# Kernel optimization log

Hardware: AMD Instinct MI355X
Metric: run time of the kernel (lower is better)

The kernel has to match this reference:

```python
import jax, jax.numpy as jnp
import numpy as np

NUM_HEADS = 16
EPS = 1e-12  # matches torch F.normalize eps


def _l2norm(t):
    n = jnp.sqrt(jnp.sum(t * t, axis=-1, keepdims=True))
    return t / jnp.maximum(n, EPS)


def setup_inputs() -> dict:
    key = jax.random.key(0)
    kx, kq, kk, kv = jax.random.split(key, 4)
    B, S, E = 2, 2048, 1024
    head_dim = E // NUM_HEADS
    bound = 1.0 / np.sqrt(E)  # nn.Linear default init range
    x = jax.random.normal(kx, (B, S, E), dtype=jnp.float32)
    Wq = jax.random.uniform(kq, (E, E), dtype=jnp.float32, minval=-bound, maxval=bound)
    Wk = jax.random.uniform(kk, (E, E), dtype=jnp.float32, minval=-bound, maxval=bound)
    Wv = jax.random.uniform(kv, (E, E), dtype=jnp.float32, minval=-bound, maxval=bound)
    g_scale = jnp.asarray(np.sqrt(head_dim), dtype=jnp.float32)  # 1/d_k = sqrt(head_dim)
    return {"x": x, "Wq": Wq, "Wk": Wk, "Wv": Wv, "g_scale": g_scale}


def reference(x, Wq, Wk, Wv, g_scale):
    B, S, E = x.shape
    H = NUM_HEADS
    D = E // H
    # projections (torch Linear: x @ W.T), split heads -> [B, H, S, D]
    q = (x @ Wq.T).reshape(B, S, H, D).transpose(0, 2, 1, 3)
    k = (x @ Wk.T).reshape(B, S, H, D).transpose(0, 2, 1, 3)
    v = (x @ Wv.T).reshape(B, S, H, D).transpose(0, 2, 1, 3)
    # qk_norm branch: L2-normalize q, k then learnable scale
    q = _l2norm(q)
    k = _l2norm(k)
    scores = g_scale * jnp.einsum('bhqd,bhkd->bhqk', q, k)  # [B, H, S, S]
    attn = jax.nn.softmax(scores, axis=-1)
    # dropout p=0.0 (eval) -> identity
    out = jnp.einsum('bhqk,bhkd->bhqd', attn, v)  # [B, H, S, D]
    out = out.transpose(0, 2, 1, 3).reshape(B, S, E)
    return out
```

## Files before the change

### kernel.cpp

```cpp
#include <hip/hip_runtime.h>
#include <math.h>

#define NH 16
#define HD 64
#define SEQ 2048
#define BAT 2
#define EMB 1024
#define MTOT (BAT*SEQ)
#define NTOT (3*EMB)

typedef __attribute__((ext_vector_type(8))) short bf16x8;
typedef __attribute__((ext_vector_type(4))) float f32x4;

#define MFMA16(a,b,c) __builtin_amdgcn_mfma_f32_16x16x32_bf16(a,b,c,0,0,0)

__device__ inline short f2bf(float f) {
    union { float f; unsigned u; } x; x.f = f;
    unsigned r = (x.u + 0x7FFF + ((x.u >> 16) & 1)) >> 16;
    return (short)r;
}

__device__ inline float fast_exp2(float x) {
#if __has_builtin(__builtin_amdgcn_exp2f)
    return __builtin_amdgcn_exp2f(x);
#else
    float r; asm("v_exp_f32 %0, %1" : "=v"(r) : "v"(x)); return r;
#endif
}

__device__ inline unsigned pack2bf_t(float a, float b) {
    union { float f; unsigned u; } x, y; x.f = a; y.f = b;
    return __builtin_amdgcn_perm(y.u, x.u, 0x07060302u);
}

typedef const __attribute__((address_space(1))) void* gp_t;
typedef __attribute__((address_space(3))) void* lp_t;
__device__ inline void gload16(const void* g, void* l) {
    __builtin_amdgcn_global_load_lds((gp_t)(uintptr_t)g, (lp_t)(uintptr_t)l, 16, 0, 0);
}

__global__ __launch_bounds__(256) void prep_kernel(
    const float* __restrict__ x, const float* __restrict__ wq,
    const float* __restrict__ wk, const float* __restrict__ wv,
    short* __restrict__ xb, short* __restrict__ wb)
{
    const size_t NX = (size_t)MTOT * EMB;
    const size_t NW = (size_t)EMB * EMB;
    const size_t i4 = ((size_t)blockIdx.x * 256 + threadIdx.x) * 4;
    float4 v; short* dst;
    if (i4 < NX) { v = *(const float4*)(x + i4); dst = xb + i4; }
    else {
        size_t j = i4 - NX;
        const float* s = (j < NW) ? wq : (j < 2 * NW) ? wk : wv;
        v = *(const float4*)(s + (j & (NW - 1)));
        dst = wb + j;
    }
    short4 o; o.x = f2bf(v.x); o.y = f2bf(v.y); o.z = f2bf(v.z); o.w = f2bf(v.w);
    *(short4*)dst = o;
}

__global__ __launch_bounds__(256) void qkv_gemm_fast(
    const short* __restrict__ xb, const short* __restrict__ wb,
    short* __restrict__ qws, short* __restrict__ kws, short* __restrict__ vperm,
    const float* __restrict__ gptr)
{
    __shared__ short smem[2 * 2 * 128 * 64];
    const int m0 = blockIdx.x * 128, n0 = blockIdx.y * 128;
    const int t = threadIdx.x, wave = t >> 6, lane = t & 63;
    const int quad = lane >> 4, l16 = lane & 15;
    const int wm = (wave & 1) * 64, wn = (wave >> 1) * 64;

    const int srow = wave * 32 + (lane >> 3);
    const int scol = ((lane & 7) ^ (srow & 7)) * 8;
    const short* ga = xb + (size_t)(m0 + srow) * EMB + scol;
    const short* gb = wb + (size_t)(n0 + srow) * EMB + scol;

    int aoff[2], boff[2];
#pragma unroll
    for (int ks = 0; ks < 2; ++ks) {
        const int pc = (ks * 32 + quad * 8) ^ ((l16 & 7) * 8);
        aoff[ks] = (wm + l16) * 64 + pc;
        boff[ks] = 8192 + (wn + l16) * 64 + pc;
    }

    f32x4 acc[4][4] = {};

    auto stageg = [&](int k0, int p) {
        short* lA = smem + p * 16384 + wave * 2048;
        short* lB = smem + p * 16384 + 8192 + wave * 2048;
#pragma unroll
        for (int j = 0; j < 4; ++j) {
            gload16(ga + k0 + (size_t)j * 8 * EMB, lA + j * 512);
            gload16(gb + k0 + (size_t)j * 8 * EMB, lB + j * 512);
        }
    };

    stageg(0, 0);
    __syncthreads();

    for (int it = 0; it < EMB / 64; ++it) {
        const int p = it & 1;
        if (it + 1 < EMB / 64) stageg((it + 1) * 64, p ^ 1);
        const short* base = smem + p * 16384;
#pragma unroll
        for (int ks = 0; ks < 2; ++ks) {
            bf16x8 af[4], bfr[4];
#pragma unroll
            for (int i = 0; i < 4; ++i) af[i]  = *(const bf16x8*)(base + aoff[ks] + i * 1024);
#pragma unroll
            for (int i = 0; i < 4; ++i) bfr[i] = *(const bf16x8*)(base + boff[ks] + i * 1024);
#pragma unroll
            for (int mf = 0; mf < 4; ++mf)
#pragma unroll
                for (int nf = 0; nf < 4; ++nf)
                    acc[mf][nf] = MFMA16(af[mf], bfr[nf], acc[mf][nf]);
        }
        __syncthreads();
    }

    short* T = smem;
    const int mat = n0 >> 10;

    if (mat < 2) {
        const float scale = (mat == 0) ? gptr[0] * 1.4426950408889634f : 1.0f;
        float inv[4][4];
#pragma unroll
        for (int mf = 0; mf < 4; ++mf)
#pragma unroll
            for (int reg = 0; reg < 4; ++reg) {
                float ss = 0.f;
#pragma unroll
                for (int nf = 0; nf < 4; ++nf) { float v = acc[mf][nf][reg]; ss += v * v; }
                ss += __shfl_xor(ss, 1, 16);
                ss += __shfl_xor(ss, 2, 16);
                ss += __shfl_xor(ss, 4, 16);
                ss += __shfl_xor(ss, 8, 16);
                inv[mf][reg] = scale / fmaxf(sqrtf(ss), 1e-12f);
            }
#pragma unroll
        for (int mf = 0; mf < 4; ++mf)
#pragma unroll
            for (int nf = 0; nf < 4; ++nf) {
                const int c = wn + nf * 16 + l16;
#pragma unroll
                for (int reg = 0; reg < 4; ++reg) {
                    const int s = wm + mf * 16 + quad * 4 + reg;
                    T[s * 128 + (((c >> 3) ^ (s & 15)) << 3) + (c & 7)] =
                        f2bf(acc[mf][nf][reg] * inv[mf][reg]);
                }
            }
        __syncthreads();
        short* outp = (mat == 0) ? qws : kws;
        const int r = t >> 1, half = t & 1;
        const int sg = m0 + r, bb = sg >> 11, sl = sg & (SEQ - 1);
        const int h = ((n0 & 1023) >> 6) + half;
        short* orow = outp + ((size_t)(bb * NH + h) * SEQ + sl) * HD;
#pragma unroll
        for (int j = 0; j < 8; ++j) {
            int4 v = *(const int4*)&T[r * 128 + ((((half * 8 + j)) ^ (r & 15)) << 3)];
            *(int4*)&orow[j * 8] = v;
        }
    } else {
#pragma unroll
        for (int mf = 0; mf < 4; ++mf)
#pragma unroll
            for (int nf = 0; nf < 4; ++nf) {
                const int c = wn + nf * 16 + l16;
#pragma unroll
                for (int reg = 0; reg < 4; ++reg) {
                    const int s = wm + mf * 16 + quad * 4 + reg;
                    const int sp = (s & ~31) + ((s & 12) >> 2) * 8 + ((s >> 4) & 1) * 4 + (s & 3);
                    T[sp * 128 + (((c >> 3) ^ (sp & 15)) << 3) + (c & 7)] =
                        f2bf(acc[mf][nf][reg]);
                }
            }
        __syncthreads();
        const int c = t >> 1, half = t & 1;
        const int h = ((n0 & 1023) >> 6) + (c >> 6), d = c & 63;
        const int bb = m0 >> 11, p0 = (m0 & (SEQ - 1)) + half * 64;
        short* vrow = vperm + ((size_t)(bb * NH + h) * HD + d) * SEQ + p0;
        const int cg = c >> 3, ce = c & 7;
#pragma unroll
        for (int j = 0; j < 8; ++j) {
            union { int4 v; short s[8]; } tmp;
#pragma unroll
            for (int e = 0; e < 8; ++e) {
                const int s = half * 64 + j * 8 + e;
                tmp.s[e] = T[s * 128 + ((cg ^ (s & 15)) << 3) + ce];
            }
            *(int4*)&vrow[j * 8] = tmp.v;
        }
    }
}

__global__ __launch_bounds__(256, 4) void attn_kernel(
    const short* __restrict__ qws, const short* __restrict__ kws,
    const short* __restrict__ vperm, float* __restrict__ out)
{
    __shared__ short Kt[2][2][2048];
    __shared__ short Vt[2][2][2048];
    __shared__ float lbuf[64];

    const int id = blockIdx.x;
    const int bh = (id & 7) * 4 + ((id >> 3) & 3);
    const int qt = id >> 5;
    const int b = bh >> 4, h = bh & (NH - 1);
    const size_t base = (size_t)bh * SEQ * HD;
    const int t = threadIdx.x, wave = t >> 6, lane = t & 63;
    const int quad = lane >> 4, l16 = lane & 15;
    const int qh = wave >> 1, kh = wave & 1;

    bf16x8 bq[2][2];
#pragma unroll
    for (int qsub = 0; qsub < 2; ++qsub) {
        const short* qp = qws + base +
            (size_t)(qt * 64 + qh * 32 + qsub * 16 + l16) * HD + quad * 8;
        bq[qsub][0] = *(const bf16x8*)(qp);
        bq[qsub][1] = *(const bf16x8*)(qp + 32);
    }
    bf16x8 ones;
#pragma unroll
    for (int i = 0; i < 8; ++i) ones[i] = (short)0x3F80;

    int koff[2][2];
#pragma unroll
    for (int msub = 0; msub < 2; ++msub)
#pragma unroll
        for (int ks = 0; ks < 2; ++ks)
            koff[msub][ks] = (msub * 16 + l16) * 64 + (((ks * 4 + quad) ^ (l16 & 7)) * 8);
    int voff[4];
#pragma unroll
    for (int nt = 0; nt < 4; ++nt) {
        const int d = nt * 16 + l16;
        voff[nt] = d * 32 + ((quad ^ ((d >> 1) & 3)) * 8);
    }

    f32x4 o_acc[2][4] = {};
    f32x4 l_acc[2] = {};

    auto stage = [&](int tt, int p) {
        if (qh == 0) {
#pragma unroll
            for (int j = 0; j < 4; ++j) {
                const int kl = j * 8 + (lane >> 3);
                const int row = tt * 64 + kh * 32 + kl;
                gload16(kws + base + (size_t)row * HD + (((lane & 7) ^ (kl & 7)) * 8),
                        &Kt[p][kh][j * 512 + lane * 8]);
            }
        } else {
#pragma unroll
            for (int j = 0; j < 4; ++j) {
                const int d = j * 16 + (lane >> 2);
                const int ug = (lane & 3) ^ ((d >> 1) & 3);
                gload16(vperm + base + (size_t)d * SEQ + tt * 64 + kh * 32 + ug * 8,
                        &Vt[p][kh][j * 512 + lane * 8]);
            }
        }
    };

    stage(0, 0);
    __syncthreads();

    for (int tt = 0; tt < SEQ / 64; ++tt) {
        const int p = tt & 1;
        if (tt + 1 < SEQ / 64) stage(tt + 1, p ^ 1);
        const short* Kp = &Kt[p][kh][0];
        const short* Vp = &Vt[p][kh][0];

        f32x4 st[2][2];
#pragma unroll
        for (int msub = 0; msub < 2; ++msub) {
            bf16x8 a0 = *(const bf16x8*)(Kp + koff[msub][0]);
            bf16x8 a1 = *(const bf16x8*)(Kp + koff[msub][1]);
#pragma unroll
            for (int qsub = 0; qsub < 2; ++qsub) {
                f32x4 z = {};
                z = MFMA16(a0, bq[qsub][0], z);
                st[msub][qsub] = MFMA16(a1, bq[qsub][1], z);
            }
        }
        bf16x8 vf[4];
#pragma unroll
        for (int nt = 0; nt < 4; ++nt)
            vf[nt] = *(const bf16x8*)(Vp + voff[nt]);
#pragma unroll
        for (int qsub = 0; qsub < 2; ++qsub) {
            bf16x8 pa;
            unsigned* pu = (unsigned*)&pa;
            pu[0] = pack2bf_t(fast_exp2(st[0][qsub][0]), fast_exp2(st[0][qsub][1]));
            pu[1] = pack2bf_t(fast_exp2(st[0][qsub][2]), fast_exp2(st[0][qsub][3]));
            pu[2] = pack2bf_t(fast_exp2(st[1][qsub][0]), fast_exp2(st[1][qsub][1]));
            pu[3] = pack2bf_t(fast_exp2(st[1][qsub][2]), fast_exp2(st[1][qsub][3]));
            l_acc[qsub] = MFMA16(pa, ones, l_acc[qsub]);
#pragma unroll
            for (int nt = 0; nt < 4; ++nt)
                o_acc[qsub][nt] = MFMA16(pa, vf[nt], o_acc[qsub][nt]);
        }
        __syncthreads();
    }

    float* red = (float*)&Kt[0][0][0];
    if (kh == 1) {
#pragma unroll
        for (int qsub = 0; qsub < 2; ++qsub) {
#pragma unroll
            for (int nt = 0; nt < 4; ++nt)
#pragma unroll
                for (int r = 0; r < 4; ++r)
                    red[qh * 2048 + (qsub * 16 + quad * 4 + r) * 64 + nt * 16 + l16] =
                        o_acc[qsub][nt][r];
            if (l16 == 0)
#pragma unroll
                for (int r = 0; r < 4; ++r)
                    lbuf[qh * 32 + qsub * 16 + quad * 4 + r] = l_acc[qsub][r];
        }
    }
    __syncthreads();
    if (kh == 0) {
#pragma unroll
        for (int qsub = 0; qsub < 2; ++qsub) {
            float linv[4];
#pragma unroll
            for (int r = 0; r < 4; ++r)
                linv[r] = 1.0f / (l_acc[qsub][r] + lbuf[qh * 32 + qsub * 16 + quad * 4 + r]);
            const int s = qt * 64 + qh * 32 + qsub * 16 + quad * 4;
            float* ob = out + ((size_t)b * SEQ + s) * EMB + h * HD + l16;
#pragma unroll
            for (int nt = 0; nt < 4; ++nt)
#pragma unroll
                for (int r = 0; r < 4; ++r) {
                    const float o = o_acc[qsub][nt][r] +
                        red[qh * 2048 + (qsub * 16 + quad * 4 + r) * 64 + nt * 16 + l16];
                    ob[(size_t)r * EMB + nt * 16] = o * linv[r];
                }
        }
    }
}

extern "C" void kernel_launch(void* const* d_in, const int* in_sizes, int n_in,
                              void* d_out, int out_size, void* d_ws, size_t ws_size,
                              hipStream_t stream) {
    (void)in_sizes; (void)n_in; (void)out_size; (void)ws_size;
    const float* x  = (const float*)d_in[0];
    const float* Wq = (const float*)d_in[1];
    const float* Wk = (const float*)d_in[2];
    const float* Wv = (const float*)d_in[3];
    const float* g  = (const float*)d_in[4];
    float* out = (float*)d_out;

    const size_t per = (size_t)BAT * NH * SEQ * HD;
    short* qws   = (short*)d_ws;
    short* kws   = qws + per;
    short* vperm = kws + per;

    short* xb = (short*)out;
    short* wb = xb + (size_t)MTOT * EMB;

    prep_kernel<<<7168, 256, 0, stream>>>(x, Wq, Wk, Wv, xb, wb);
    qkv_gemm_fast<<<dim3(MTOT / 128, NTOT / 128), 256, 0, stream>>>(
        xb, wb, qws, kws, vperm, g);
    attn_kernel<<<(SEQ / 64) * BAT * NH, 256, 0, stream>>>(qws, kws, vperm, out);
}
```

Baseline: 161.6 us.

## Store bf16 operands in MFMA fragment-native tiled layout across all kernels

Changes the prep kernel, the QKV GEMM epilogue and the attention kernel so that x, weights, Q, K and V are stored in 16x32 fragment-blocked tiles matching the MFMA operand lane order. Global-to-LDS staging and LDS fragment reads then become plain contiguous lane*8 accesses, with no XOR swizzle or per-row address arithmetic. The goal is fewer address computations and fully contiguous 1KB loads. The cost is that LDS reads lose the swizzle and may hit bank conflicts, and the V epilogue scatter becomes more complex.

```diff
diff --git a/kernel.cpp b/kernel.cpp
--- a/kernel.cpp
+++ b/kernel.cpp
@@ -39,24 +39,33 @@
     __builtin_amdgcn_global_load_lds((gp_t)(uintptr_t)g, (lp_t)(uintptr_t)l, 16, 0, 0);
 }
 
+
 __global__ __launch_bounds__(256) void prep_kernel(
     const float* __restrict__ x, const float* __restrict__ wq,
     const float* __restrict__ wk, const float* __restrict__ wv,
     short* __restrict__ xb, short* __restrict__ wb)
 {
-    const size_t NX = (size_t)MTOT * EMB;
-    const size_t NW = (size_t)EMB * EMB;
-    const size_t i4 = ((size_t)blockIdx.x * 256 + threadIdx.x) * 4;
-    float4 v; short* dst;
-    if (i4 < NX) { v = *(const float4*)(x + i4); dst = xb + i4; }
-    else {
-        size_t j = i4 - NX;
-        const float* s = (j < NW) ? wq : (j < 2 * NW) ? wk : wv;
-        v = *(const float4*)(s + (j & (NW - 1)));
-        dst = wb + j;
-    }
-    short4 o; o.x = f2bf(v.x); o.y = f2bf(v.y); o.z = f2bf(v.z); o.w = f2bf(v.w);
-    *(short4*)dst = o;
+    const int g = blockIdx.x * 256 + threadIdx.x;
+    const int bid = g >> 6, lane = g & 63;
+    const int l16 = lane & 15, quad = lane >> 4;
+    const float* src; short* dst;
+    if (bid < 8192) {
+        const int S = bid >> 5, kb = bid & 31;
+        src = x + (size_t)(S * 16 + l16) * EMB + kb * 32 + quad * 8;
+        dst = xb + (size_t)bid * 512 + lane * 8;
+    } else {
+        const int wid = bid - 8192;
+        const int mat = wid >> 11, within = wid & 2047;
+        const int S = within >> 5, kb = within & 31;
+        const float* w = (mat == 0) ? wq : (mat == 1) ? wk : wv;
+        src = w + (size_t)(S * 16 + l16) * EMB + kb * 32 + quad * 8;
+        dst = wb + (size_t)wid * 512 + lane * 8;
+    }
+    float4 a = *(const float4*)src, b2 = *(const float4*)(src + 4);
+    union { int4 v; short s[8]; } o;
+    o.s[0]=f2bf(a.x);  o.s[1]=f2bf(a.y);  o.s[2]=f2bf(a.z);  o.s[3]=f2bf(a.w);
+    o.s[4]=f2bf(b2.x); o.s[5]=f2bf(b2.y); o.s[6]=f2bf(b2.z); o.s[7]=f2bf(b2.w);
+    *(int4*)dst = o.v;
 }
 
 __global__ __launch_bounds__(256) void qkv_gemm_fast(
@@ -64,34 +73,36 @@
     short* __restrict__ qws, short* __restrict__ kws, short* __restrict__ vperm,
     const float* __restrict__ gptr)
 {
-    __shared__ short smem[2 * 2 * 128 * 64];
+    __shared__ short smem[2 * 16384];
     const int m0 = blockIdx.x * 128, n0 = blockIdx.y * 128;
     const int t = threadIdx.x, wave = t >> 6, lane = t & 63;
     const int quad = lane >> 4, l16 = lane & 15;
     const int wm = (wave & 1) * 64, wn = (wave >> 1) * 64;
-
-    const int srow = wave * 32 + (lane >> 3);
-    const int scol = ((lane & 7) ^ (srow & 7)) * 8;
-    const short* ga = xb + (size_t)(m0 + srow) * EMB + scol;
-    const short* gb = wb + (size_t)(n0 + srow) * EMB + scol;
+    const int SA = m0 >> 4;
+    const int SB = n0 >> 4;
 
     int aoff[2], boff[2];
 #pragma unroll
     for (int ks = 0; ks < 2; ++ks) {
-        const int pc = (ks * 32 + quad * 8) ^ ((l16 & 7) * 8);
-        aoff[ks] = (wm + l16) * 64 + pc;
-        boff[ks] = 8192 + (wn + l16) * 64 + pc;
+        aoff[ks] = ((wave & 1) * 8 + ks) * 512 + lane * 8;
+        boff[ks] = 8192 + ((wave >> 1) * 8 + ks) * 512 + lane * 8;
     }
 
     f32x4 acc[4][4] = {};
 
-    auto stageg = [&](int k0, int p) {
-        short* lA = smem + p * 16384 + wave * 2048;
-        short* lB = smem + p * 16384 + 8192 + wave * 2048;
-#pragma unroll
-        for (int j = 0; j < 4; ++j) {
-            gload16(ga + k0 + (size_t)j * 8 * EMB, lA + j * 512);
-            gload16(gb + k0 + (size_t)j * 8 * EMB, lB + j * 512);
+    auto stageg = [&](int it, int p) {
+        short* ls = smem + p * 16384;
+        const int kb0 = it * 2;
+#pragma unroll
+        for (int s = 0; s < 2; ++s) {
+            const int sg = wave * 2 + s;
+#pragma unroll
+            for (int kbl = 0; kbl < 2; ++kbl) {
+                gload16(xb + ((size_t)(SA + sg) * 32 + kb0 + kbl) * 512 + lane * 8,
+                        ls + (sg * 2 + kbl) * 512 + lane * 8);
+                gload16(wb + ((size_t)(SB + sg) * 32 + kb0 + kbl) * 512 + lane * 8,
+                        ls + 8192 + (sg * 2 + kbl) * 512 + lane * 8);
+            }
         }
     };
 
@@ -100,7 +111,7 @@
 
     for (int it = 0; it < EMB / 64; ++it) {
         const int p = it & 1;
-        if (it + 1 < EMB / 64) stageg((it + 1) * 64, p ^ 1);
+        if (it + 1 < EMB / 64) stageg(it + 1, p ^ 1);
         const short* base = smem + p * 16384;
 #pragma unroll
         for (int ks = 0; ks < 2; ++ks) {
@@ -154,11 +165,11 @@
         const int r = t >> 1, half = t & 1;
         const int sg = m0 + r, bb = sg >> 11, sl = sg & (SEQ - 1);
         const int h = ((n0 & 1023) >> 6) + half;
-        short* orow = outp + ((size_t)(bb * NH + h) * SEQ + sl) * HD;
+        short* obase = outp + ((size_t)(bb * NH + h) * 128 + (sl >> 4)) * 1024;
 #pragma unroll
         for (int j = 0; j < 8; ++j) {
-            int4 v = *(const int4*)&T[r * 128 + ((((half * 8 + j)) ^ (r & 15)) << 3)];
-            *(int4*)&orow[j * 8] = v;
+            int4 v = *(const int4*)&T[r * 128 + (((half * 8 + j) ^ (r & 15)) << 3)];
+            *(int4*)&obase[(j >> 2) * 512 + ((j & 3) * 16 + (sl & 15)) * 8] = v;
         }
     } else {
 #pragma unroll
@@ -169,26 +180,31 @@
 #pragma unroll
                 for (int reg = 0; reg < 4; ++reg) {
                     const int s = wm + mf * 16 + quad * 4 + reg;
-                    const int sp = (s & ~31) + ((s & 12) >> 2) * 8 + ((s >> 4) & 1) * 4 + (s & 3);
-                    T[sp * 128 + (((c >> 3) ^ (sp & 15)) << 3) + (c & 7)] =
+                    T[s * 128 + (((c >> 3) ^ (s & 15)) << 3) + (c & 7)] =
                         f2bf(acc[mf][nf][reg]);
                 }
             }
         __syncthreads();
         const int c = t >> 1, half = t & 1;
         const int h = ((n0 & 1023) >> 6) + (c >> 6), d = c & 63;
-        const int bb = m0 >> 11, p0 = (m0 & (SEQ - 1)) + half * 64;
-        short* vrow = vperm + ((size_t)(bb * NH + h) * HD + d) * SEQ + p0;
+        const int nt = d >> 4, l16v = d & 15;
+        const int bb = m0 >> 11, sl0 = m0 & (SEQ - 1);
         const int cg = c >> 3, ce = c & 7;
 #pragma unroll
-        for (int j = 0; j < 8; ++j) {
-            union { int4 v; short s[8]; } tmp;
-#pragma unroll
-            for (int e = 0; e < 8; ++e) {
-                const int s = half * 64 + j * 8 + e;
-                tmp.s[e] = T[s * 128 + ((cg ^ (s & 15)) << 3) + ce];
-            }
-            *(int4*)&vrow[j * 8] = tmp.v;
+        for (int ss = 0; ss < 2; ++ss) {
+            const int strip = (sl0 >> 5) + half * 2 + ss;
+            short* vb = vperm + (((size_t)(bb * NH + h) * 64 + strip) * 4 + nt) * 512;
+#pragma unroll
+            for (int q = 0; q < 4; ++q) {
+                union { int4 v; short s[8]; } tmp;
+#pragma unroll
+                for (int jj = 0; jj < 8; ++jj) {
+                    const int tl = (jj & 3) | (((jj >> 2) & 1) << 4) | (q << 2);
+                    const int row = half * 64 + ss * 32 + tl;
+                    tmp.s[jj] = T[row * 128 + ((cg ^ (row & 15)) << 3) + ce];
+                }
+                *(int4*)&vb[(q * 16 + l16v) * 8] = tmp.v;
+            }
         }
     }
 }
@@ -205,7 +221,6 @@
     const int bh = (id & 7) * 4 + ((id >> 3) & 3);
     const int qt = id >> 5;
     const int b = bh >> 4, h = bh & (NH - 1);
-    const size_t base = (size_t)bh * SEQ * HD;
     const int t = threadIdx.x, wave = t >> 6, lane = t & 63;
     const int quad = lane >> 4, l16 = lane & 15;
     const int qh = wave >> 1, kh = wave & 1;
@@ -213,48 +228,33 @@
     bf16x8 bq[2][2];
 #pragma unroll
     for (int qsub = 0; qsub < 2; ++qsub) {
-        const short* qp = qws + base +
-            (size_t)(qt * 64 + qh * 32 + qsub * 16 + l16) * HD + quad * 8;
+        const short* qp = qws +
+            ((size_t)bh * 128 + qt * 4 + qh * 2 + qsub) * 1024 + lane * 8;
         bq[qsub][0] = *(const bf16x8*)(qp);
-        bq[qsub][1] = *(const bf16x8*)(qp + 32);
+        bq[qsub][1] = *(const bf16x8*)(qp + 512);
     }
     bf16x8 ones;
 #pragma unroll
     for (int i = 0; i < 8; ++i) ones[i] = (short)0x3F80;
-
-    int koff[2][2];
-#pragma unroll
-    for (int msub = 0; msub < 2; ++msub)
-#pragma unroll
-        for (int ks = 0; ks < 2; ++ks)
-            koff[msub][ks] = (msub * 16 + l16) * 64 + (((ks * 4 + quad) ^ (l16 & 7)) * 8);
-    int voff[4];
-#pragma unroll
-    for (int nt = 0; nt < 4; ++nt) {
-        const int d = nt * 16 + l16;
-        voff[nt] = d * 32 + ((quad ^ ((d >> 1) & 3)) * 8);
-    }
 
     f32x4 o_acc[2][4] = {};
     f32x4 l_acc[2] = {};
 
     auto stage = [&](int tt, int p) {
         if (qh == 0) {
-#pragma unroll
-            for (int j = 0; j < 4; ++j) {
-                const int kl = j * 8 + (lane >> 3);
-                const int row = tt * 64 + kh * 32 + kl;
-                gload16(kws + base + (size_t)row * HD + (((lane & 7) ^ (kl & 7)) * 8),
-                        &Kt[p][kh][j * 512 + lane * 8]);
-            }
+            const size_t kb = (size_t)bh * 128 + tt * 4 + kh * 2;
+#pragma unroll
+            for (int s = 0; s < 2; ++s)
+#pragma unroll
+                for (int ks = 0; ks < 2; ++ks)
+                    gload16(kws + ((kb + s) * 2 + ks) * 512 + lane * 8,
+                            &Kt[p][kh][(s * 2 + ks) * 512 + lane * 8]);
         } else {
-#pragma unroll
-            for (int j = 0; j < 4; ++j) {
-                const int d = j * 16 + (lane >> 2);
-                const int ug = (lane & 3) ^ ((d >> 1) & 3);
-                gload16(vperm + base + (size_t)d * SEQ + tt * 64 + kh * 32 + ug * 8,
-                        &Vt[p][kh][j * 512 + lane * 8]);
-            }
+            const size_t vb = ((size_t)bh * 64 + tt * 2 + kh) * 4;
+#pragma unroll
+            for (int nt = 0; nt < 4; ++nt)
+                gload16(vperm + (vb + nt) * 512 + lane * 8,
+                        &Vt[p][kh][nt * 512 + lane * 8]);
         }
     };
 
@@ -270,8 +270,8 @@
         f32x4 st[2][2];
 #pragma unroll
         for (int msub = 0; msub < 2; ++msub) {
-            bf16x8 a0 = *(const bf16x8*)(Kp + koff[msub][0]);
-            bf16x8 a1 = *(const bf16x8*)(Kp + koff[msub][1]);
+            bf16x8 a0 = *(const bf16x8*)(Kp + (msub * 2 + 0) * 512 + lane * 8);
+            bf16x8 a1 = *(const bf16x8*)(Kp + (msub * 2 + 1) * 512 + lane * 8);
 #pragma unroll
             for (int qsub = 0; qsub < 2; ++qsub) {
                 f32x4 z = {};
@@ -282,7 +282,7 @@
         bf16x8 vf[4];
 #pragma unroll
         for (int nt = 0; nt < 4; ++nt)
-            vf[nt] = *(const bf16x8*)(Vp + voff[nt]);
+            vf[nt] = *(const bf16x8*)(Vp + nt * 512 + lane * 8);
 #pragma unroll
         for (int qsub = 0; qsub < 2; ++qsub) {
             bf16x8 pa;
@@ -356,7 +356,7 @@
     short* xb = (short*)out;
     short* wb = xb + (size_t)MTOT * EMB;
 
-    prep_kernel<<<7168, 256, 0, stream>>>(x, Wq, Wk, Wv, xb, wb);
+    prep_kernel<<<3584, 256, 0, stream>>>(x, Wq, Wk, Wv, xb, wb);
     qkv_gemm_fast<<<dim3(MTOT / 128, NTOT / 128), 256, 0, stream>>>(
         xb, wb, qws, kws, vperm, g);
     attn_kernel<<<(SEQ / 64) * BAT * NH, 256, 0, stream>>>(qws, kws, vperm, out);
```

After: 162.2 us. About the same (+0.3%).
